# Kernel optimization log

Hardware: AMD Instinct MI355X
Metric: run time of the kernel (lower is better)

Reference implementation:

```python
import jax, jax.numpy as jnp
import numpy as np

B, N, C, K, OUT = 4, 10000, 128, 16, 128


def setup_inputs() -> dict:
    key = jax.random.key(0)
    k1, k2, k3, k4 = jax.random.split(key, 4)
    x = jax.random.normal(k1, (B, N, C), dtype=jnp.float32)
    edge_index = jax.random.randint(k2, (2, B, N, K), 0, N)
    # Linear(2C -> OUT), torch convention W: [OUT, 2C]
    W = jax.random.normal(k3, (OUT, 2 * C), dtype=jnp.float32) * 0.05
    b = jax.random.normal(k4, (OUT,), dtype=jnp.float32) * 0.05
    return {"x": x, "edge_index": edge_index, "W": W, "b": b}


def reference(x, edge_index, W, b):
    # x: [B, N, C] -> [B, C, N]
    xt = jnp.swapaxes(x, 1, 2)
    Bs, Cs, Ns = xt.shape
    # batched_index_select: [C, N] gathered by [N, K] -> [C, N, K], vmapped over batch
    gather = jax.vmap(lambda xb, ib: xb[:, ib])
    x_i = gather(xt, edge_index[1])  # [B, C, N, K]
    x_j = gather(xt, edge_index[0])  # [B, C, N, K]
    rel = jnp.max(x_j - x_i, axis=-1)  # max-relative: [B, C, N]
    # interleave channels: [x_0, rel_0, x_1, rel_1, ...] -> [B, 2C, N]
    feat = jnp.stack([xt, rel], axis=2).reshape(Bs, 2 * Cs, Ns)
    feat = jnp.swapaxes(feat, 1, 2)  # [B, N, 2C]
    out = feat @ W.T + b  # Linear(2C -> OUT)
    return jax.nn.relu(out)
```

## Files before the change

### kernel.cpp

```cpp
#include <hip/hip_runtime.h>


#define Bn 4
#define Nn 10000
#define Cn 128
#define Kn 16
#define OUTn 128
#define Mn 16
#define FPAD 8

typedef __attribute__((ext_vector_type(8))) short short8;
typedef __attribute__((ext_vector_type(4))) float floatx4;

__device__ __forceinline__ unsigned short f2bf(float f) {
    union { float f; unsigned u; } v; v.f = f;
    unsigned r = v.u + 0x7fffu + ((v.u >> 16) & 1u);
    return (unsigned short)(r >> 16);
}

__global__ __launch_bounds__(256) void build_wb(const float* __restrict__ W,
                                                unsigned short* __restrict__ Wb) {
    int tid = blockIdx.x * 256 + threadIdx.x;
    int lane = tid & 63;
    int step = (tid >> 6) & 7;
    int tile = tid >> 9;
    int o = tile * 16 + (lane & 15);
    int quad = lane >> 4;
    unsigned short v[8];
#pragma unroll
    for (int j = 0; j < 8; ++j) {
        int c2 = step * 32 + quad * 8 + j;
        v[j] = f2bf(W[o * (2 * Cn) + c2]);
    }
    uint4 pk;
    pk.x = (unsigned)v[0] | ((unsigned)v[1] << 16);
    pk.y = (unsigned)v[2] | ((unsigned)v[3] << 16);
    pk.z = (unsigned)v[4] | ((unsigned)v[5] << 16);
    pk.w = (unsigned)v[6] | ((unsigned)v[7] << 16);
    *(uint4*)(Wb + (size_t)tid * 8) = pk;
}

__global__ __launch_bounds__(256) void mrconv_kernel(
    const float* __restrict__ x, const int* __restrict__ edge,
    const unsigned short* __restrict__ Wb, const float* __restrict__ bias,
    float* __restrict__ out)
{
    __shared__ unsigned short sfeat[Mn][2 * Cn + FPAD];
    __shared__ int sidx[2][Mn][Kn];

    int bi = blockIdx.x;
    int slot = bi & 7;
    int b = slot & 3;
    int nb = (bi >> 3) * 2 + (slot >> 2);
    if (nb >= Nn / Mn) return;
    const int n0 = nb * Mn;
    const int gbase = b * Nn + n0;

    const int t = threadIdx.x;
    const int wv = t >> 6;
    const int lane = t & 63;

    for (int i = t; i < 2 * Mn * Kn; i += 256) {
        int s = i >> 8;
        int m = (i >> 4) & 15;
        int k = i & 15;
        sidx[s][m][k] = edge[s * (Bn * Nn * Kn) + (gbase + m) * Kn + k];
    }
    __syncthreads();

    const float* xb = x + b * (Nn * Cn);

    const int half = lane >> 5;
    const int ch = 4 * (lane & 31);
    for (int pr = 0; pr < 2; ++pr) {
        const int m = wv * 4 + pr * 2 + half;
        const float4 xs = *(const float4*)(xb + (n0 + m) * Cn + ch);
        float4 r = {-3.402823466e+38f, -3.402823466e+38f,
                    -3.402823466e+38f, -3.402823466e+38f};
#pragma unroll
        for (int kc = 0; kc < 2; ++kc) {
            float4 vj[8], vi[8];
#pragma unroll
            for (int u = 0; u < 8; ++u) {
                const int jj = sidx[0][m][kc * 8 + u];
                const int ii = sidx[1][m][kc * 8 + u];
                vj[u] = *(const float4*)(xb + jj * Cn + ch);
                vi[u] = *(const float4*)(xb + ii * Cn + ch);
            }
#pragma unroll
            for (int u = 0; u < 8; ++u) {
                r.x = fmaxf(r.x, vj[u].x - vi[u].x);
                r.y = fmaxf(r.y, vj[u].y - vi[u].y);
                r.z = fmaxf(r.z, vj[u].z - vi[u].z);
                r.w = fmaxf(r.w, vj[u].w - vi[u].w);
            }
        }
        uint4 pk;
        pk.x = (unsigned)f2bf(xs.x) | ((unsigned)f2bf(r.x) << 16);
        pk.y = (unsigned)f2bf(xs.y) | ((unsigned)f2bf(r.y) << 16);
        pk.z = (unsigned)f2bf(xs.z) | ((unsigned)f2bf(r.z) << 16);
        pk.w = (unsigned)f2bf(xs.w) | ((unsigned)f2bf(r.w) << 16);
        *(uint4*)&sfeat[m][2 * ch] = pk;
    }
    __syncthreads();

    const int m16 = lane & 15;
    const int quad = lane >> 4;
    floatx4 acc0 = {0.f, 0.f, 0.f, 0.f};
    floatx4 acc1 = {0.f, 0.f, 0.f, 0.f};
    const short8* wb8 = (const short8*)Wb;
    const int tile0 = 2 * wv, tile1 = 2 * wv + 1;
#pragma unroll
    for (int step = 0; step < 8; ++step) {
        short8 a = *(const short8*)&sfeat[m16][step * 32 + quad * 8];
        short8 b0 = wb8[(tile0 * 8 + step) * 64 + lane];
        short8 b1 = wb8[(tile1 * 8 + step) * 64 + lane];
        acc0 = __builtin_amdgcn_mfma_f32_16x16x32_bf16(a, b0, acc0, 0, 0, 0);
        acc1 = __builtin_amdgcn_mfma_f32_16x16x32_bf16(a, b1, acc1, 0, 0, 0);
    }
    const int o0 = tile0 * 16 + m16;
    const int o1 = tile1 * 16 + m16;
    const float bb0 = bias[o0], bb1 = bias[o1];
#pragma unroll
    for (int r = 0; r < 4; ++r) {
        int g = gbase + quad * 4 + r;
        out[g * OUTn + o0] = fmaxf(acc0[r] + bb0, 0.f);
        out[g * OUTn + o1] = fmaxf(acc1[r] + bb1, 0.f);
    }
}

extern "C" void kernel_launch(void* const* d_in, const int* in_sizes, int n_in,
                              void* d_out, int out_size, void* d_ws, size_t ws_size,
                              hipStream_t stream) {
    const float* x = (const float*)d_in[0];
    const int* edge = (const int*)d_in[1];
    const float* W = (const float*)d_in[2];
    const float* bias = (const float*)d_in[3];
    float* out = (float*)d_out;
    unsigned short* Wb = (unsigned short*)d_ws;

    build_wb<<<16, 256, 0, stream>>>(W, Wb);
    mrconv_kernel<<<2560, 256, 0, stream>>>(x, edge, Wb, bias, out);
}
```

Before: 113.1 us.

## Convert x to fp16 up front and gather half-precision rows with packed max

A new prep kernel converts x (and W) to fp16 in workspace, so the gather phase reads half-width rows. Each lane now handles 8 channels with packed fp16 subtract and max, and the GEMM switches from bf16 to fp16 MFMA. This aims to halve the random-gather traffic, which dominates, at the cost of an extra pass over x and fp16 rounding in the max-relative differences.

```diff
diff --git a/kernel.cpp b/kernel.cpp
--- a/kernel.cpp
+++ b/kernel.cpp
@@ -9,43 +9,47 @@
 #define Mn 16
 #define FPAD 8
 
-typedef __attribute__((ext_vector_type(8))) short short8;
-typedef __attribute__((ext_vector_type(4))) float floatx4;
+typedef _Float16 half8v __attribute__((ext_vector_type(8)));
+typedef float floatx4 __attribute__((ext_vector_type(4)));
 
-__device__ __forceinline__ unsigned short f2bf(float f) {
-    union { float f; unsigned u; } v; v.f = f;
-    unsigned r = v.u + 0x7fffu + ((v.u >> 16) & 1u);
-    return (unsigned short)(r >> 16);
+__global__ __launch_bounds__(256) void prep(const float* __restrict__ x,
+                                            const float* __restrict__ W,
+                                            _Float16* __restrict__ xh,
+                                            _Float16* __restrict__ Wh) {
+    if (blockIdx.x < 2500) {
+        int i = blockIdx.x * 256 + threadIdx.x;
+        const float4* x4 = (const float4*)x;
+        float4 a = x4[2 * i];
+        float4 c = x4[2 * i + 1];
+        union { _Float16 h[8]; uint4 q; } pk;
+        pk.h[0] = (_Float16)a.x; pk.h[1] = (_Float16)a.y;
+        pk.h[2] = (_Float16)a.z; pk.h[3] = (_Float16)a.w;
+        pk.h[4] = (_Float16)c.x; pk.h[5] = (_Float16)c.y;
+        pk.h[6] = (_Float16)c.z; pk.h[7] = (_Float16)c.w;
+        *(uint4*)(xh + 8 * (size_t)i) = pk.q;
+    } else {
+        int tid = (blockIdx.x - 2500) * 256 + threadIdx.x;
+        int lane = tid & 63;
+        int step = (tid >> 6) & 7;
+        int tile = tid >> 9;
+        int o = tile * 16 + (lane & 15);
+        int quad = lane >> 4;
+        union { _Float16 h[8]; uint4 q; } pk;
+#pragma unroll
+        for (int j = 0; j < 8; ++j) {
+            int c2 = step * 32 + quad * 8 + j;
+            pk.h[j] = (_Float16)W[o * (2 * Cn) + c2];
+        }
+        *(uint4*)(Wh + (size_t)tid * 8) = pk.q;
+    }
 }
 
-__global__ __launch_bounds__(256) void build_wb(const float* __restrict__ W,
-                                                unsigned short* __restrict__ Wb) {
-    int tid = blockIdx.x * 256 + threadIdx.x;
-    int lane = tid & 63;
-    int step = (tid >> 6) & 7;
-    int tile = tid >> 9;
-    int o = tile * 16 + (lane & 15);
-    int quad = lane >> 4;
-    unsigned short v[8];
-#pragma unroll
-    for (int j = 0; j < 8; ++j) {
-        int c2 = step * 32 + quad * 8 + j;
-        v[j] = f2bf(W[o * (2 * Cn) + c2]);
-    }
-    uint4 pk;
-    pk.x = (unsigned)v[0] | ((unsigned)v[1] << 16);
-    pk.y = (unsigned)v[2] | ((unsigned)v[3] << 16);
-    pk.z = (unsigned)v[4] | ((unsigned)v[5] << 16);
-    pk.w = (unsigned)v[6] | ((unsigned)v[7] << 16);
-    *(uint4*)(Wb + (size_t)tid * 8) = pk;
-}
-
-__global__ __launch_bounds__(256) void mrconv_kernel(
-    const float* __restrict__ x, const int* __restrict__ edge,
-    const unsigned short* __restrict__ Wb, const float* __restrict__ bias,
+__global__ __launch_bounds__(256, 4) void mrconv_kernel(
+    const _Float16* __restrict__ xh, const int* __restrict__ edge,
+    const _Float16* __restrict__ Wh, const float* __restrict__ bias,
     float* __restrict__ out)
 {
-    __shared__ unsigned short sfeat[Mn][2 * Cn + FPAD];
+    __shared__ _Float16 sfeat[Mn][2 * Cn + FPAD];
     __shared__ int sidx[2][Mn][Kn];
 
     int bi = blockIdx.x;
@@ -68,39 +72,41 @@
     }
     __syncthreads();
 
-    const float* xb = x + b * (Nn * Cn);
+    const _Float16* xbb = xh + (size_t)b * Nn * Cn;
 
-    const int half = lane >> 5;
-    const int ch = 4 * (lane & 31);
-    for (int pr = 0; pr < 2; ++pr) {
-        const int m = wv * 4 + pr * 2 + half;
-        const float4 xs = *(const float4*)(xb + (n0 + m) * Cn + ch);
-        float4 r = {-3.402823466e+38f, -3.402823466e+38f,
-                    -3.402823466e+38f, -3.402823466e+38f};
+    {
+        const int q = lane >> 4;
+        const int l16 = lane & 15;
+        const int m = wv * 4 + q;
+        const int ch = l16 * 8;
+        const half8v xs = *(const half8v*)(xbb + (n0 + m) * Cn + ch);
+        half8v r;
+#pragma unroll
+        for (int e = 0; e < 8; ++e) r[e] = (_Float16)(-65504.0f);
 #pragma unroll
         for (int kc = 0; kc < 2; ++kc) {
-            float4 vj[8], vi[8];
+            half8v vj[8], vi[8];
 #pragma unroll
             for (int u = 0; u < 8; ++u) {
                 const int jj = sidx[0][m][kc * 8 + u];
                 const int ii = sidx[1][m][kc * 8 + u];
-                vj[u] = *(const float4*)(xb + jj * Cn + ch);
-                vi[u] = *(const float4*)(xb + ii * Cn + ch);
+                vj[u] = *(const half8v*)(xbb + jj * Cn + ch);
+                vi[u] = *(const half8v*)(xbb + ii * Cn + ch);
             }
 #pragma unroll
             for (int u = 0; u < 8; ++u) {
-                r.x = fmaxf(r.x, vj[u].x - vi[u].x);
-                r.y = fmaxf(r.y, vj[u].y - vi[u].y);
-                r.z = fmaxf(r.z, vj[u].z - vi[u].z);
-                r.w = fmaxf(r.w, vj[u].w - vi[u].w);
+                half8v d = vj[u] - vi[u];
+                r = __builtin_elementwise_max(r, d);
             }
         }
-        uint4 pk;
-        pk.x = (unsigned)f2bf(xs.x) | ((unsigned)f2bf(r.x) << 16);
-        pk.y = (unsigned)f2bf(xs.y) | ((unsigned)f2bf(r.y) << 16);
-        pk.z = (unsigned)f2bf(xs.z) | ((unsigned)f2bf(r.z) << 16);
-        pk.w = (unsigned)f2bf(xs.w) | ((unsigned)f2bf(r.w) << 16);
-        *(uint4*)&sfeat[m][2 * ch] = pk;
+        union { _Float16 h[16]; uint4 q[2]; } pk;
+#pragma unroll
+        for (int e = 0; e < 8; ++e) {
+            pk.h[2 * e] = xs[e];
+            pk.h[2 * e + 1] = r[e];
+        }
+        *(uint4*)&sfeat[m][2 * ch] = pk.q[0];
+        *(uint4*)&sfeat[m][2 * ch + 8] = pk.q[1];
     }
     __syncthreads();
 
@@ -108,15 +114,15 @@
     const int quad = lane >> 4;
     floatx4 acc0 = {0.f, 0.f, 0.f, 0.f};
     floatx4 acc1 = {0.f, 0.f, 0.f, 0.f};
-    const short8* wb8 = (const short8*)Wb;
+    const half8v* wh8 = (const half8v*)Wh;
     const int tile0 = 2 * wv, tile1 = 2 * wv + 1;
 #pragma unroll
     for (int step = 0; step < 8; ++step) {
-        short8 a = *(const short8*)&sfeat[m16][step * 32 + quad * 8];
-        short8 b0 = wb8[(tile0 * 8 + step) * 64 + lane];
-        short8 b1 = wb8[(tile1 * 8 + step) * 64 + lane];
-        acc0 = __builtin_amdgcn_mfma_f32_16x16x32_bf16(a, b0, acc0, 0, 0, 0);
-        acc1 = __builtin_amdgcn_mfma_f32_16x16x32_bf16(a, b1, acc1, 0, 0, 0);
+        half8v a = *(const half8v*)&sfeat[m16][step * 32 + quad * 8];
+        half8v b0 = wh8[(tile0 * 8 + step) * 64 + lane];
+        half8v b1 = wh8[(tile1 * 8 + step) * 64 + lane];
+        acc0 = __builtin_amdgcn_mfma_f32_16x16x32_f16(a, b0, acc0, 0, 0, 0);
+        acc1 = __builtin_amdgcn_mfma_f32_16x16x32_f16(a, b1, acc1, 0, 0, 0);
     }
     const int o0 = tile0 * 16 + m16;
     const int o1 = tile1 * 16 + m16;
@@ -137,8 +143,10 @@
     const float* W = (const float*)d_in[2];
     const float* bias = (const float*)d_in[3];
     float* out = (float*)d_out;
-    unsigned short* Wb = (unsigned short*)d_ws;
 
-    build_wb<<<16, 256, 0, stream>>>(W, Wb);
-    mrconv_kernel<<<2560, 256, 0, stream>>>(x, edge, Wb, bias, out);
+    _Float16* Wh = (_Float16*)d_ws;
+    _Float16* xh = (_Float16*)((char*)d_ws + 65536);
+
+    prep<<<2516, 256, 0, stream>>>(x, W, xh, Wh);
+    mrconv_kernel<<<2560, 256, 0, stream>>>(xh, edge, Wh, bias, out);
 }
```

Result: faster. 102.7 us (-9.2%).
